# Optimization experiments

Hardware: AMD Instinct MI355X
Metric: run time of the kernel (lower is better)

Reference implementation:

```python
import jax, jax.numpy as jnp
import numpy as np

N_VIEWS = 8


def _trilinear(vol, pts):
    """Trilinear interpolation of vol [Nx,Ny,Nz] at pts [...,3] (voxel coords), zero outside."""
    nx, ny, nz = vol.shape
    x, y, z = pts[..., 0], pts[..., 1], pts[..., 2]
    x0f, y0f, z0f = jnp.floor(x), jnp.floor(y), jnp.floor(z)
    fx, fy, fz = x - x0f, y - y0f, z - z0f
    x0 = x0f.astype(jnp.int32)
    y0 = y0f.astype(jnp.int32)
    z0 = z0f.astype(jnp.int32)
    out = jnp.zeros(x.shape, vol.dtype)
    for dx in (0, 1):
        wx = fx if dx else (1.0 - fx)
        ix = x0 + dx
        vx = (ix >= 0) & (ix < nx)
        ixc = jnp.clip(ix, 0, nx - 1)
        for dy in (0, 1):
            wy = fy if dy else (1.0 - fy)
            iy = y0 + dy
            vxy = vx & (iy >= 0) & (iy < ny)
            iyc = jnp.clip(iy, 0, ny - 1)
            for dz in (0, 1):
                wz = fz if dz else (1.0 - fz)
                iz = z0 + dz
                valid = vxy & (iz >= 0) & (iz < nz)
                izc = jnp.clip(iz, 0, nz - 1)
                v = vol[ixc, iyc, izc]  # irregular gather
                out = out + jnp.where(valid, v, jnp.zeros((), vol.dtype)) * (wx * wy * wz)
    return out


def cone_project(vol, src_pos, det_center, det_u_vec, det_v_vec,
                 det_u, det_v, du, dv, voxel_spacing, n_steps):
    """Cone-beam forward projection: ray-march src->detector pixel, trilinear sampling."""
    nx, ny, nz = vol.shape
    us = (jnp.arange(det_u, dtype=vol.dtype) - (det_u - 1) / 2.0) * du
    vs = (jnp.arange(det_v, dtype=vol.dtype) - (det_v - 1) / 2.0) * dv
    # detector pixel world positions: [V, U, W, 3]
    det_pts = (det_center[:, None, None, :]
               + us[None, :, None, None] * det_u_vec[:, None, None, :]
               + vs[None, None, :, None] * det_v_vec[:, None, None, :])
    src = src_pos[:, None, None, :]            # [V,1,1,3]
    diff = det_pts - src                        # [V,U,W,3]
    ray_len = jnp.sqrt(jnp.sum(diff * diff, axis=-1))  # [V,U,W]
    step_len = ray_len / n_steps
    center = (jnp.array([nx, ny, nz], dtype=vol.dtype) - 1.0) / 2.0
    fracs = (jnp.arange(n_steps, dtype=vol.dtype) + 0.5) / n_steps

    def body(acc, s):
        p = src + s * diff                      # world coords [V,U,W,3]
        vox = p / voxel_spacing + center        # voxel coords
        return acc + _trilinear(vol, vox), None

    acc, _ = jax.lax.scan(body, jnp.zeros(ray_len.shape, vol.dtype), fracs)
    return acc * step_len


def setup_inputs() -> dict:
    key = jax.random.key(0)
    k1, k2 = jax.random.split(key)
    vol_shape = (256, 256, 256)
    x = 0.1 * jax.random.normal(k1, vol_shape, dtype=jnp.float32)
    reco = 0.1 * jax.random.normal(k2, vol_shape, dtype=jnp.float32)
    # circular cone-beam trajectory (units = voxels, spacing 1.0)
    sad, sdd = 400.0, 800.0  # source-axis / source-detector distance
    angles = np.linspace(0.0, np.pi, N_VIEWS, endpoint=False)
    ca, sa = np.cos(angles), np.sin(angles)
    zeros = np.zeros(N_VIEWS)
    src_pos = np.stack([-sad * ca, -sad * sa, zeros], axis=-1)
    det_center = np.stack([(sdd - sad) * ca, (sdd - sad) * sa, zeros], axis=-1)
    det_u_vec = np.stack([-sa, ca, zeros], axis=-1)
    det_v_vec = np.tile(np.array([0.0, 0.0, 1.0]), (N_VIEWS, 1))
    return {
        "x": x,
        "reco": reco,
        "src_pos": jnp.asarray(src_pos, jnp.float32),
        "det_center": jnp.asarray(det_center, jnp.float32),
        "det_u_vec": jnp.asarray(det_u_vec, jnp.float32),
        "det_v_vec": jnp.asarray(det_v_vec, jnp.float32),
        "du": 3.0,
        "dv": 3.0,
        "voxel_spacing": 1.0,
        "det_u": 128,
        "det_v": 128,
        "n_steps": 192,
    }


def reference(x, reco, src_pos, det_center, det_u_vec, det_v_vec,
              du, dv, voxel_spacing, det_u, det_v, n_steps):
    updated = x + reco
    sino = cone_project(updated, src_pos, det_center, det_u_vec, det_v_vec,
                        det_u, det_v, du, dv, voxel_spacing, n_steps)
    return sino, jax.nn.relu(updated)
```

## Files before the change

### kernel.cpp

```cpp
#include <hip/hip_runtime.h>
#include <math.h>

typedef float nfloat4 __attribute__((ext_vector_type(4)));

__global__ __launch_bounds__(256) void add_relu_kernel(
    const float* __restrict__ x,
    const float* __restrict__ reco,
    float* __restrict__ relu_out,
    float* __restrict__ upd_out,
    int n4)
{
    int i = blockIdx.x * blockDim.x + threadIdx.x;
    int stride = gridDim.x * blockDim.x;
    const nfloat4* x4 = (const nfloat4*)x;
    const nfloat4* r4 = (const nfloat4*)reco;
    nfloat4* ro4 = (nfloat4*)relu_out;
    nfloat4* uo4 = (nfloat4*)upd_out;
    for (; i < n4; i += stride) {
        nfloat4 a = x4[i];
        nfloat4 b = r4[i];
        nfloat4 u = a + b;
        if (uo4) uo4[i] = u;
        nfloat4 r;
        r.x = fmaxf(u.x, 0.f); r.y = fmaxf(u.y, 0.f);
        r.z = fmaxf(u.z, 0.f); r.w = fmaxf(u.w, 0.f);
        ro4[i] = r;
    }
}

template <int TWO>
__device__ __forceinline__ float fetch_corner(
    const float* __restrict__ vol_a,
    const float* __restrict__ vol_b,
    int ix, int iy, int iz,
    int nx, int ny, int nz)
{
    bool valid = (ix >= 0) & (ix < nx) & (iy >= 0) & (iy < ny) &
                 (iz >= 0) & (iz < nz);
    if (!valid) return 0.0f;
    int idx = (ix * ny + iy) * nz + iz;
    float v = vol_a[idx];
    if (TWO) v += vol_b[idx];
    return v;
}

__device__ __forceinline__ void clip_axis(float a, float b, float lo, float hi,
                                          float& t_lo, float& t_hi)
{
    if (fabsf(b) > 1e-6f) {
        float t0 = (lo - a) / b;
        float t1 = (hi - a) / b;
        float tmn = fminf(t0, t1);
        float tmx = fmaxf(t0, t1);
        t_lo = fmaxf(t_lo, tmn);
        t_hi = fminf(t_hi, tmx);
    } else {
        if (a <= lo || a >= hi) { t_lo = 1.0f; t_hi = 0.0f; }
    }
}

template <int TWO>
__global__ __launch_bounds__(256) void cone_project_seg_kernel(
    const float* __restrict__ vol_a,
    const float* __restrict__ vol_b,
    const float* __restrict__ src_pos,
    const float* __restrict__ det_center,
    const float* __restrict__ det_u_vec,
    const float* __restrict__ det_v_vec,
    const float* __restrict__ du_p,
    const float* __restrict__ dv_p,
    const float* __restrict__ spacing_p,
    const int* __restrict__ det_u_p,
    const int* __restrict__ det_v_p,
    const int* __restrict__ nsteps_p,
    float* __restrict__ sino,
    int n_views, int nx, int ny, int nz)
{
    const int det_u = *det_u_p;
    const int det_v = *det_v_p;
    const int n_steps = *nsteps_p;
    const float du = *du_p;
    const float dv = *dv_p;
    const float inv_sp = 1.0f / *spacing_p;

    const long total = (long)n_views * det_u * det_v;
    const int pix = threadIdx.x & 63;
    const int seg = threadIdx.x >> 6;
    const long idx = (long)blockIdx.x * 64 + pix;
    const bool live = idx < total;

    const long cidx = live ? idx : 0;
    const int v = (int)(cidx % det_v);
    const int u = (int)((cidx / det_v) % det_u);
    const int view = (int)(cidx / ((long)det_u * det_v));

    const float us = ((float)u - (det_u - 1) * 0.5f) * du;
    const float vs = ((float)v - (det_v - 1) * 0.5f) * dv;

    const float sx = src_pos[view * 3 + 0];
    const float sy = src_pos[view * 3 + 1];
    const float sz = src_pos[view * 3 + 2];

    const float dpx = det_center[view * 3 + 0] + us * det_u_vec[view * 3 + 0] + vs * det_v_vec[view * 3 + 0];
    const float dpy = det_center[view * 3 + 1] + us * det_u_vec[view * 3 + 1] + vs * det_v_vec[view * 3 + 1];
    const float dpz = det_center[view * 3 + 2] + us * det_u_vec[view * 3 + 2] + vs * det_v_vec[view * 3 + 2];

    const float dx = dpx - sx;
    const float dy = dpy - sy;
    const float dz = dpz - sz;
    const float ray_len = sqrtf(dx * dx + dy * dy + dz * dz);
    const float step_len = ray_len / (float)n_steps;

    const float cx = (nx - 1) * 0.5f;
    const float cy = (ny - 1) * 0.5f;
    const float cz = (nz - 1) * 0.5f;

    float t_lo = 0.0f, t_hi = 1.0f;
    clip_axis(sx * inv_sp + cx, dx * inv_sp, -1.0f, (float)nx, t_lo, t_hi);
    clip_axis(sy * inv_sp + cy, dy * inv_sp, -1.0f, (float)ny, t_lo, t_hi);
    clip_axis(sz * inv_sp + cz, dz * inv_sp, -1.0f, (float)nz, t_lo, t_hi);

    int i_min = 0, i_max = -1;
    if (t_hi > t_lo) {
        i_min = (int)floorf(t_lo * (float)n_steps - 0.5f) - 1;
        i_max = (int)ceilf(t_hi * (float)n_steps - 0.5f) + 1;
        i_min = max(i_min, 0);
        i_max = min(i_max, n_steps - 1);
    }
    if (!live) { i_min = 0; i_max = -1; }

    const int count = i_max - i_min + 1;
    const int per = (count + 3) >> 2;
    const int is = i_min + seg * per;
    const int ie = min(is + per - 1, i_max);

    const float inv_n = 1.0f / (float)n_steps;
    const int snz = ny * nz;

    float acc = 0.0f;
    for (int i = is; i <= ie; ++i) {
        const float s = ((float)i + 0.5f) * inv_n;
        const float px = fmaf(s, dx, sx) * inv_sp + cx;
        const float py = fmaf(s, dy, sy) * inv_sp + cy;
        const float pz = fmaf(s, dz, sz) * inv_sp + cz;

        const float x0f = floorf(px);
        const float y0f = floorf(py);
        const float z0f = floorf(pz);
        const float fx = px - x0f;
        const float fy = py - y0f;
        const float fz = pz - z0f;
        const int x0 = (int)x0f;
        const int y0 = (int)y0f;
        const int z0 = (int)z0f;

        const float gx = 1.0f - fx;
        const float gy = 1.0f - fy;
        const float gz = 1.0f - fz;

        const bool interior = (x0 >= 0) & (x0 + 1 < nx) &
                              (y0 >= 0) & (y0 + 1 < ny) &
                              (z0 >= 0) & (z0 + 1 < nz);

        float samp = 0.0f;
        if (interior) {
            const int base = (x0 * ny + y0) * nz + z0;
            const float* pa = vol_a + base;
            float v000 = pa[0];
            float v001 = pa[1];
            float v010 = pa[nz];
            float v011 = pa[nz + 1];
            float v100 = pa[snz];
            float v101 = pa[snz + 1];
            float v110 = pa[snz + nz];
            float v111 = pa[snz + nz + 1];
            if (TWO) {
                const float* pb = vol_b + base;
                v000 += pb[0];
                v001 += pb[1];
                v010 += pb[nz];
                v011 += pb[nz + 1];
                v100 += pb[snz];
                v101 += pb[snz + 1];
                v110 += pb[snz + nz];
                v111 += pb[snz + nz + 1];
            }
            samp = fmaf(gx * gy * gz, v000, samp);
            samp = fmaf(gx * gy * fz, v001, samp);
            samp = fmaf(gx * fy * gz, v010, samp);
            samp = fmaf(gx * fy * fz, v011, samp);
            samp = fmaf(fx * gy * gz, v100, samp);
            samp = fmaf(fx * gy * fz, v101, samp);
            samp = fmaf(fx * fy * gz, v110, samp);
            samp = fmaf(fx * fy * fz, v111, samp);
        } else {
            samp = fmaf(gx * gy * gz, fetch_corner<TWO>(vol_a, vol_b, x0,     y0,     z0,     nx, ny, nz), samp);
            samp = fmaf(gx * gy * fz, fetch_corner<TWO>(vol_a, vol_b, x0,     y0,     z0 + 1, nx, ny, nz), samp);
            samp = fmaf(gx * fy * gz, fetch_corner<TWO>(vol_a, vol_b, x0,     y0 + 1, z0,     nx, ny, nz), samp);
            samp = fmaf(gx * fy * fz, fetch_corner<TWO>(vol_a, vol_b, x0,     y0 + 1, z0 + 1, nx, ny, nz), samp);
            samp = fmaf(fx * gy * gz, fetch_corner<TWO>(vol_a, vol_b, x0 + 1, y0,     z0,     nx, ny, nz), samp);
            samp = fmaf(fx * gy * fz, fetch_corner<TWO>(vol_a, vol_b, x0 + 1, y0,     z0 + 1, nx, ny, nz), samp);
            samp = fmaf(fx * fy * gz, fetch_corner<TWO>(vol_a, vol_b, x0 + 1, y0 + 1, z0,     nx, ny, nz), samp);
            samp = fmaf(fx * fy * fz, fetch_corner<TWO>(vol_a, vol_b, x0 + 1, y0 + 1, z0 + 1, nx, ny, nz), samp);
        }
        acc += samp;
    }

    __shared__ float red[256];
    red[threadIdx.x] = acc;
    __syncthreads();
    if (seg == 0 && live) {
        float tot = red[pix] + red[pix + 64] + red[pix + 128] + red[pix + 192];
        sino[idx] = tot * step_len;
    }
}

extern "C" void kernel_launch(void* const* d_in, const int* in_sizes, int n_in,
                              void* d_out, int out_size, void* d_ws, size_t ws_size,
                              hipStream_t stream) {
    const float* x          = (const float*)d_in[0];
    const float* reco       = (const float*)d_in[1];
    const float* src_pos    = (const float*)d_in[2];
    const float* det_center = (const float*)d_in[3];
    const float* det_u_vec  = (const float*)d_in[4];
    const float* det_v_vec  = (const float*)d_in[5];
    const float* du_p       = (const float*)d_in[6];
    const float* dv_p       = (const float*)d_in[7];
    const float* spacing_p  = (const float*)d_in[8];
    const int*   det_u_p    = (const int*)d_in[9];
    const int*   det_v_p    = (const int*)d_in[10];
    const int*   nsteps_p   = (const int*)d_in[11];

    const int n_vol = in_sizes[0];
    const int n_views = in_sizes[2] / 3;

    int n = 1;
    while ((long)(n + 1) * (n + 1) * (n + 1) <= (long)n_vol) ++n;
    const int nx = n, ny = n, nz = n;

    const int sino_size = out_size - n_vol;
    float* sino     = (float*)d_out;
    float* relu_out = (float*)d_out + sino_size;

    const bool use_ws = ws_size >= (size_t)n_vol * sizeof(float);
    float* upd = (float*)d_ws;

    const int n4 = n_vol / 4;
    add_relu_kernel<<<2048, 256, 0, stream>>>(
        x, reco, relu_out, use_ws ? upd : nullptr, n4);

    const int blocks = (sino_size + 63) / 64;
    if (use_ws) {
        cone_project_seg_kernel<0><<<blocks, 256, 0, stream>>>(
            upd, nullptr,
            src_pos, det_center, det_u_vec, det_v_vec,
            du_p, dv_p, spacing_p, det_u_p, det_v_p, nsteps_p,
            sino, n_views, nx, ny, nz);
    } else {
        cone_project_seg_kernel<1><<<blocks, 256, 0, stream>>>(
            x, reco,
            src_pos, det_center, det_u_vec, det_v_vec,
            du_p, dv_p, spacing_p, det_u_p, det_v_p, nsteps_p,
            sino, n_views, nx, ny, nz);
    }
}
```

Before: 237.0 us.

## Split add from relu and co-schedule relu blocks inside projection kernel

The first kernel now only writes x+reco to the workspace. The relu output is computed by blocks interleaved into the projection grid, so the memory-bound relu store can overlap with the gather-heavy ray marching. This takes the relu write off the critical path before projection starts, but the relu pass now rereads upd, adding a volume read and some block scheduling overhead.

```diff
diff --git a/kernel.cpp b/kernel.cpp
--- a/kernel.cpp
+++ b/kernel.cpp
@@ -3,11 +3,26 @@
 
 typedef float nfloat4 __attribute__((ext_vector_type(4)));
 
-__global__ __launch_bounds__(256) void add_relu_kernel(
+__global__ __launch_bounds__(256) void add_stage_kernel(
+    const float* __restrict__ x,
+    const float* __restrict__ reco,
+    float* __restrict__ upd_out,
+    int n4)
+{
+    int i = blockIdx.x * blockDim.x + threadIdx.x;
+    int stride = gridDim.x * blockDim.x;
+    const nfloat4* x4 = (const nfloat4*)x;
+    const nfloat4* r4 = (const nfloat4*)reco;
+    nfloat4* uo4 = (nfloat4*)upd_out;
+    for (; i < n4; i += stride) {
+        uo4[i] = x4[i] + r4[i];
+    }
+}
+
+__global__ __launch_bounds__(256) void add_relu_only_kernel(
     const float* __restrict__ x,
     const float* __restrict__ reco,
     float* __restrict__ relu_out,
-    float* __restrict__ upd_out,
     int n4)
 {
     int i = blockIdx.x * blockDim.x + threadIdx.x;
@@ -15,12 +30,8 @@
     const nfloat4* x4 = (const nfloat4*)x;
     const nfloat4* r4 = (const nfloat4*)reco;
     nfloat4* ro4 = (nfloat4*)relu_out;
-    nfloat4* uo4 = (nfloat4*)upd_out;
     for (; i < n4; i += stride) {
-        nfloat4 a = x4[i];
-        nfloat4 b = r4[i];
-        nfloat4 u = a + b;
-        if (uo4) uo4[i] = u;
+        nfloat4 u = x4[i] + r4[i];
         nfloat4 r;
         r.x = fmaxf(u.x, 0.f); r.y = fmaxf(u.y, 0.f);
         r.z = fmaxf(u.z, 0.f); r.w = fmaxf(u.w, 0.f);
@@ -60,7 +71,8 @@
 }
 
 template <int TWO>
-__global__ __launch_bounds__(256) void cone_project_seg_kernel(
+__device__ __forceinline__ void proj_block_body(
+    int pb,
     const float* __restrict__ vol_a,
     const float* __restrict__ vol_b,
     const float* __restrict__ src_pos,
@@ -86,7 +98,7 @@
     const long total = (long)n_views * det_u * det_v;
     const int pix = threadIdx.x & 63;
     const int seg = threadIdx.x >> 6;
-    const long idx = (long)blockIdx.x * 64 + pix;
+    const long idx = (long)pb * 64 + pix;
     const bool live = idx < total;
 
     const long cidx = live ? idx : 0;
@@ -175,15 +187,15 @@
             float v110 = pa[snz + nz];
             float v111 = pa[snz + nz + 1];
             if (TWO) {
-                const float* pb = vol_b + base;
-                v000 += pb[0];
-                v001 += pb[1];
-                v010 += pb[nz];
-                v011 += pb[nz + 1];
-                v100 += pb[snz];
-                v101 += pb[snz + 1];
-                v110 += pb[snz + nz];
-                v111 += pb[snz + nz + 1];
+                const float* pb2 = vol_b + base;
+                v000 += pb2[0];
+                v001 += pb2[1];
+                v010 += pb2[nz];
+                v011 += pb2[nz + 1];
+                v100 += pb2[snz];
+                v101 += pb2[snz + 1];
+                v110 += pb2[snz + nz];
+                v111 += pb2[snz + nz + 1];
             }
             samp = fmaf(gx * gy * gz, v000, samp);
             samp = fmaf(gx * gy * fz, v001, samp);
@@ -215,6 +227,72 @@
     }
 }
 
+__global__ __launch_bounds__(256) void relu_proj_kernel(
+    const float* __restrict__ upd,
+    float* __restrict__ relu_out,
+    const float* __restrict__ src_pos,
+    const float* __restrict__ det_center,
+    const float* __restrict__ det_u_vec,
+    const float* __restrict__ det_v_vec,
+    const float* __restrict__ du_p,
+    const float* __restrict__ dv_p,
+    const float* __restrict__ spacing_p,
+    const int* __restrict__ det_u_p,
+    const int* __restrict__ det_v_p,
+    const int* __restrict__ nsteps_p,
+    float* __restrict__ sino,
+    int n4, int relu_blocks,
+    int n_views, int nx, int ny, int nz)
+{
+    const int b = blockIdx.x;
+    const int total_b = gridDim.x;
+    const long relu_before = ((long)b * relu_blocks) / total_b;
+    const bool is_relu = (((long)(b + 1) * relu_blocks) / total_b) > relu_before;
+
+    if (is_relu) {
+        const int rid = (int)relu_before;
+        const nfloat4* u4 = (const nfloat4*)upd;
+        nfloat4* ro4 = (nfloat4*)relu_out;
+        int i = rid * 256 + threadIdx.x;
+        const int stride = relu_blocks * 256;
+        for (; i < n4; i += stride) {
+            nfloat4 u = u4[i];
+            nfloat4 r;
+            r.x = fmaxf(u.x, 0.f); r.y = fmaxf(u.y, 0.f);
+            r.z = fmaxf(u.z, 0.f); r.w = fmaxf(u.w, 0.f);
+            ro4[i] = r;
+        }
+        return;
+    }
+
+    proj_block_body<0>((int)(b - relu_before), upd, nullptr,
+                       src_pos, det_center, det_u_vec, det_v_vec,
+                       du_p, dv_p, spacing_p, det_u_p, det_v_p, nsteps_p,
+                       sino, n_views, nx, ny, nz);
+}
+
+__global__ __launch_bounds__(256) void cone_project_fallback_kernel(
+    const float* __restrict__ x,
+    const float* __restrict__ reco,
+    const float* __restrict__ src_pos,
+    const float* __restrict__ det_center,
+    const float* __restrict__ det_u_vec,
+    const float* __restrict__ det_v_vec,
+    const float* __restrict__ du_p,
+    const float* __restrict__ dv_p,
+    const float* __restrict__ spacing_p,
+    const int* __restrict__ det_u_p,
+    const int* __restrict__ det_v_p,
+    const int* __restrict__ nsteps_p,
+    float* __restrict__ sino,
+    int n_views, int nx, int ny, int nz)
+{
+    proj_block_body<1>(blockIdx.x, x, reco,
+                       src_pos, det_center, det_u_vec, det_v_vec,
+                       du_p, dv_p, spacing_p, det_u_p, det_v_p, nsteps_p,
+                       sino, n_views, nx, ny, nz);
+}
+
 extern "C" void kernel_launch(void* const* d_in, const int* in_sizes, int n_in,
                               void* d_out, int out_size, void* d_ws, size_t ws_size,
                               hipStream_t stream) {
@@ -246,18 +324,20 @@
     float* upd = (float*)d_ws;
 
     const int n4 = n_vol / 4;
-    add_relu_kernel<<<2048, 256, 0, stream>>>(
-        x, reco, relu_out, use_ws ? upd : nullptr, n4);
-
-    const int blocks = (sino_size + 63) / 64;
+    const int proj_blocks = (sino_size + 63) / 64;
+
     if (use_ws) {
-        cone_project_seg_kernel<0><<<blocks, 256, 0, stream>>>(
-            upd, nullptr,
+        add_stage_kernel<<<2048, 256, 0, stream>>>(x, reco, upd, n4);
+
+        const int relu_blocks = 2048;
+        relu_proj_kernel<<<relu_blocks + proj_blocks, 256, 0, stream>>>(
+            upd, relu_out,
             src_pos, det_center, det_u_vec, det_v_vec,
             du_p, dv_p, spacing_p, det_u_p, det_v_p, nsteps_p,
-            sino, n_views, nx, ny, nz);
+            sino, n4, relu_blocks, n_views, nx, ny, nz);
     } else {
-        cone_project_seg_kernel<1><<<blocks, 256, 0, stream>>>(
+        add_relu_only_kernel<<<2048, 256, 0, stream>>>(x, reco, relu_out, n4);
+        cone_project_fallback_kernel<<<proj_blocks, 256, 0, stream>>>(
             x, reco,
             src_pos, det_center, det_u_vec, det_v_vec,
             du_p, dv_p, spacing_p, det_u_p, det_v_p, nsteps_p,
```

Measured after the change: 239.8 us. About the same (+1.2%).
